# Kernel tuning notes

Hardware: AMD Instinct MI355X
Metric: run time of the kernel (lower is better)

## Reference

```python
import jax, jax.numpy as jnp
import numpy as np
import math

B, T, D, H = 2, 2048, 768, 12
ND = D // H  # head dim = 64


def precompute_freqs_cis(dim, end, theta=10000.0):
    freqs = 1.0 / (theta ** (jnp.arange(0, dim, 2, dtype=jnp.float32) / dim))  # [dim/2]
    t = jnp.arange(end, dtype=jnp.float32)
    freqs = jnp.outer(t, freqs)  # [end, dim/2]
    return jnp.cos(freqs), jnp.sin(freqs)


def apply_rotary_emb(q, k, cos, sin):
    # q, k: [b, t, h, nd]; cos/sin: [t, nd/2]
    def rot(x):
        xr, xi = x[..., 0::2], x[..., 1::2]  # even/odd interleaved split
        c = cos[None, :, None, :]
        s = sin[None, :, None, :]
        out_r = xr * c - xi * s
        out_i = xr * s + xi * c
        return jnp.stack([out_r, out_i], axis=-1).reshape(x.shape)
    return rot(q), rot(k)


def setup_inputs() -> dict:
    key = jax.random.key(0)
    ks = jax.random.split(key, 12)
    sc = 0.02
    q = jax.random.normal(ks[0], (B, T, D), dtype=jnp.float32)
    k = jax.random.normal(ks[1], (B, T, D), dtype=jnp.float32)
    v = jax.random.normal(ks[2], (B, T, D), dtype=jnp.float32)
    mask = jnp.tril(jnp.ones((T, T), dtype=jnp.int32))[None, None]  # causal [1,1,T,T]
    # weights stored as [d_in, d_out] (pre-transposed vs torch Linear)
    wq = jax.random.normal(ks[3], (D, D), dtype=jnp.float32) * sc
    bq = jax.random.normal(ks[4], (D,), dtype=jnp.float32) * sc
    wk = jax.random.normal(ks[5], (D, D), dtype=jnp.float32) * sc
    bk = jax.random.normal(ks[6], (D,), dtype=jnp.float32) * sc
    wv = jax.random.normal(ks[7], (D, D), dtype=jnp.float32) * sc
    bv = jax.random.normal(ks[8], (D,), dtype=jnp.float32) * sc
    wo = jax.random.normal(ks[9], (D, D), dtype=jnp.float32) * sc
    cos, sin = precompute_freqs_cis(ND, T)
    return {"q": q, "k": k, "v": v, "mask": mask, "wq": wq, "bq": bq,
            "wk": wk, "bk": bk, "wv": wv, "bv": bv, "wo": wo,
            "freqs_cos": cos, "freqs_sin": sin}


def reference(q, k, v, mask, wq, bq, wk, bk, wv, bv, wo, freqs_cos, freqs_sin):
    b, t, d = q.shape
    qh = (q @ wq + bq).reshape(b, t, H, ND)
    kh = (k @ wk + bk).reshape(b, t, H, ND)
    vh = (v @ wv + bv).reshape(b, t, H, ND).transpose(0, 2, 1, 3)  # [b,h,t,nd]
    qh, kh = apply_rotary_emb(qh, kh, freqs_cos[:t], freqs_sin[:t])
    qh = qh.transpose(0, 2, 1, 3)  # [b,h,t,nd]
    kh = kh.transpose(0, 2, 1, 3)
    attn = jnp.einsum('bhqd,bhkd->bhqk', qh, kh) / math.sqrt(ND)
    attn = jnp.where(mask == 0, jnp.float32(-jnp.inf), attn)
    probs = jax.nn.softmax(attn, axis=-1)
    out = jnp.einsum('bhqk,bhkd->bhqd', probs, vh)
    out = out.transpose(0, 2, 1, 3).reshape(b, t, d)
    return out @ wo
```

## Files before the change

### kernel.cpp

```cpp
#include <hip/hip_runtime.h>
#include <hip/hip_bf16.h>
#include <math.h>

#define BB 2
#define TT 2048
#define DD 768
#define HH 12
#define ND 64
#define MM (BB*TT)

typedef __attribute__((ext_vector_type(8))) short bf16x8;
typedef __attribute__((ext_vector_type(4))) float f32x4;
typedef __attribute__((ext_vector_type(16))) float f32x16;

__device__ __forceinline__ float bf2f(ushort u) {
    union { unsigned int i; float f; } v; v.i = ((unsigned int)u) << 16; return v.f;
}
__device__ __forceinline__ ushort f2bf(float f) {
    union { float f; unsigned int i; } v; v.f = f;
    unsigned int r = v.i + 0x7FFF + ((v.i >> 16) & 1);
    return (ushort)(r >> 16);
}

__device__ __forceinline__ void cp16(void* lds, const void* g) {
    __builtin_amdgcn_global_load_lds(
        (const __attribute__((address_space(1))) void*)g,
        (__attribute__((address_space(3))) void*)lds, 16, 0, 0);
}

__device__ __forceinline__ float fexp2(float x) {
    float r; asm("v_exp_f32 %0, %1" : "=v"(r) : "v"(x)); return r;
}
__device__ __forceinline__ unsigned int pk_bf16(float a, float b) {
    unsigned int r; asm("v_cvt_pk_bf16_f32 %0, %1, %2" : "=v"(r) : "v"(a), "v"(b)); return r;
}

__device__ __forceinline__ void plswap(unsigned int& a, unsigned int& b) {
#if __has_builtin(__builtin_amdgcn_permlane32_swap)
    auto r = __builtin_amdgcn_permlane32_swap(a, b, false, false);
    a = r[0]; b = r[1];
#else
    unsigned int sa = __shfl_xor((int)a, 32), sb = __shfl_xor((int)b, 32);
    bool hi = (threadIdx.x & 63) >= 32;
    unsigned int na = hi ? sb : a, nb = hi ? b : sa;
    a = na; b = nb;
#endif
}
__device__ __forceinline__ float partner32(float x, int hi) {
#if __has_builtin(__builtin_amdgcn_permlane32_swap)
    unsigned int u = __float_as_uint(x);
    auto r = __builtin_amdgcn_permlane32_swap(u, u, false, false);
    return __uint_as_float(hi ? r[0] : r[1]);
#else
    return __shfl_xor(x, 32);
#endif
}

#define QSCALE 0.18033688011112043f

__global__ void conv_x3(const float* __restrict__ x0, const float* __restrict__ x1,
                        const float* __restrict__ x2,
                        ushort* __restrict__ o0, ushort* __restrict__ o1,
                        ushort* __restrict__ o2)
{
    const float* x = blockIdx.z == 0 ? x0 : (blockIdx.z == 1 ? x1 : x2);
    ushort* o = blockIdx.z == 0 ? o0 : (blockIdx.z == 1 ? o1 : o2);
    int i = (blockIdx.x * 256 + threadIdx.x) * 4;
    if (i >= MM * DD) return;
    float4 v = *(const float4*)&x[i];
    ushort4 r;
    r.x = f2bf(v.x); r.y = f2bf(v.y); r.z = f2bf(v.z); r.w = f2bf(v.w);
    *(ushort4*)&o[i] = r;
}

__global__ __launch_bounds__(256) void conv_wT(const float* __restrict__ w0, const float* __restrict__ w1,
                        const float* __restrict__ w2, const float* __restrict__ w3,
                        ushort* __restrict__ o0, ushort* __restrict__ o1,
                        ushort* __restrict__ o2, ushort* __restrict__ o3)
{
    __shared__ ushort tile[64][72];
    const float* w = blockIdx.z == 0 ? w0 : blockIdx.z == 1 ? w1 : blockIdx.z == 2 ? w2 : w3;
    ushort* o = blockIdx.z == 0 ? o0 : blockIdx.z == 1 ? o1 : blockIdx.z == 2 ? o2 : o3;
    const int k0 = blockIdx.y * 64, n0 = blockIdx.x * 64;
    #pragma unroll
    for (int it = 0; it < 4; ++it) {
        int e = (threadIdx.x + it * 256) * 4;
        int r = e >> 6, c = e & 63;
        float4 v = *(const float4*)&w[(size_t)(k0 + r) * DD + n0 + c];
        tile[c + 0][r] = f2bf(v.x);
        tile[c + 1][r] = f2bf(v.y);
        tile[c + 2][r] = f2bf(v.z);
        tile[c + 3][r] = f2bf(v.w);
    }
    __syncthreads();
    #pragma unroll
    for (int it = 0; it < 4; ++it) {
        int e = (threadIdx.x + it * 256) * 4;
        int nr = e >> 6, kc = e & 63;
        ushort4 r4;
        r4.x = tile[nr][kc + 0];
        r4.y = tile[nr][kc + 1];
        r4.z = tile[nr][kc + 2];
        r4.w = tile[nr][kc + 3];
        *(ushort4*)&o[(size_t)(n0 + nr) * DD + k0 + kc] = r4;
    }
}

struct GArgs { const ushort* x; const ushort* wt; const float* bias; void* out;
               const float* cT; const float* sT; int rope; };

template<int MODE, int TM, int TN>
__global__ __launch_bounds__(256) void gemm_bf16(GArgs a0, GArgs a1, GArgs a2,
                                                 int nx, int ny)
{
    constexpr int WM = TM / 2, WN = TN / 2;
    constexpr int MF = WM / 16, NF = WN / 16;
    constexpr int BUFB = (TM + TN) * 64;
    constexpr int NPASS = BUFB / 4096;
    constexpr int NK = DD / 32;
    __shared__ __align__(16) ushort S[3][BUFB / 2];
    const int tid = threadIdx.x;
    const int w = tid >> 6, l = tid & 63;
    const int wr = w >> 1, wc = w & 1;

    const int G = gridDim.x, per = G >> 3;
    const int p = blockIdx.x;
    const int task = (p & 7) * per + (p >> 3);
    const int bx = task % nx;
    const int by = (task / nx) % ny;
    const int bz = task / (nx * ny);
    GArgs ga = (bz == 0) ? a0 : (bz == 1 ? a1 : a2);
    const int n0 = bx * TN, m0 = by * TM;

    f32x4 acc[MF][NF] = {};

    auto stage = [&](int buf, int k0) {
        #pragma unroll
        for (int it = 0; it < NPASS; ++it) {
            const int ob = it * 4096 + w * 1024;
            const int o = ob + l * 16;
            if (ob < TM * 64) {
                const int row = o >> 6, kb = o & 63;
                cp16((char*)&S[buf][0] + ob,
                     (const char*)ga.x + (size_t)(m0 + row) * (DD * 2) + k0 * 2 + kb);
            } else {
                const int o2 = o - TM * 64;
                const int row = o2 >> 6, kb = o2 & 63;
                cp16((char*)&S[buf][0] + ob,
                     (const char*)ga.wt + (size_t)(n0 + row) * (DD * 2) + k0 * 2 + kb);
            }
        }
    };

    stage(0, 0);
    stage(1, 32);
    if constexpr (NPASS == 2) asm volatile("s_waitcnt vmcnt(2)" ::: "memory");
    else                      asm volatile("s_waitcnt vmcnt(3)" ::: "memory");
    __builtin_amdgcn_s_barrier();

    for (int t = 0; t < NK; ++t) {
        const bool more = (t + 2 < NK);
        if (more) stage((t + 2) % 3, (t + 2) * 32);

        const char* ab = (const char*)&S[t % 3][0];
        bf16x8 af[MF], bfr[NF];
        #pragma unroll
        for (int i = 0; i < MF; ++i)
            af[i] = *(const bf16x8*)(ab + (WM * wr + 16 * i + (l & 15)) * 64 + (l >> 4) * 16);
        #pragma unroll
        for (int j = 0; j < NF; ++j)
            bfr[j] = *(const bf16x8*)(ab + TM * 64 + (WN * wc + 16 * j + (l & 15)) * 64 + (l >> 4) * 16);
        __builtin_amdgcn_s_setprio(1);
        #pragma unroll
        for (int i = 0; i < MF; ++i)
            #pragma unroll
            for (int j = 0; j < NF; ++j)
                acc[i][j] = __builtin_amdgcn_mfma_f32_16x16x32_bf16(af[i], bfr[j], acc[i][j], 0, 0, 0);
        __builtin_amdgcn_s_setprio(0);

        if (more) {
            if constexpr (NPASS == 2) asm volatile("s_waitcnt vmcnt(2)" ::: "memory");
            else                      asm volatile("s_waitcnt vmcnt(3)" ::: "memory");
        } else {
            asm volatile("s_waitcnt vmcnt(0)" ::: "memory");
        }
        __builtin_amdgcn_s_barrier();
    }
    asm volatile("s_waitcnt vmcnt(0)" ::: "memory");

    #pragma unroll
    for (int i = 0; i < MF; ++i) {
        #pragma unroll
        for (int j = 0; j < NF; ++j) {
            #pragma unroll
            for (int r = 0; r < 4; ++r) {
                const int m = m0 + WM * wr + 16 * i + (l >> 4) * 4 + r;
                const int n = n0 + WN * wc + 16 * j + (l & 15);
                float v = acc[i][j][r];
                if (MODE == 0) {
                    v += ga.bias[n];
                    const int tt = m & 2047;
                    if (ga.rope) {
                        const int d = n & 63;
                        const float c = ga.cT[tt * 32 + (d >> 1)];
                        const float s = ga.sT[tt * 32 + (d >> 1)];
                        const float pv = __shfl_xor(v, 1);
                        v = (n & 1) ? (pv * s + v * c) : (v * c - pv * s);
                        if (ga.rope == 2) v *= QSCALE;
                    }
                    const int b = m >> 11;
                    const int h = n >> 6, d = n & 63;
                    ((ushort*)ga.out)[((size_t)(b * HH + h) * TT + tt) * ND + d] = f2bf(v);
                } else {
                    ((float*)ga.out)[(size_t)m * DD + n] = v;
                }
            }
        }
    }
}

__global__ __launch_bounds__(256) void transpose_v(const ushort* __restrict__ Vh,
                                                   ushort* __restrict__ VhT)
{
    __shared__ ushort tile[64][72];
    const int t0 = blockIdx.x * 64, bh = blockIdx.y;
    const ushort* src = Vh + ((size_t)bh * TT + t0) * ND;
    #pragma unroll
    for (int it = 0; it < 4; ++it) {
        int e = (threadIdx.x + it * 256) * 4;
        int r = e >> 6, c = e & 63;
        ushort4 v = *(const ushort4*)&src[r * ND + c];
        tile[r][c + 0] = v.x; tile[r][c + 1] = v.y;
        tile[r][c + 2] = v.z; tile[r][c + 3] = v.w;
    }
    __syncthreads();
    #pragma unroll
    for (int it = 0; it < 4; ++it) {
        int e = (threadIdx.x + it * 256) * 4;
        int d = e >> 6, tc = e & 63;
        ushort4 r4;
        r4.x = tile[tc + 0][d]; r4.y = tile[tc + 1][d];
        r4.z = tile[tc + 2][d]; r4.w = tile[tc + 3][d];
        *(ushort4*)&VhT[((size_t)bh * ND + d) * TT + t0 + tc] = r4;
    }
}

#define NQB (TT/128)
#define NBH (BB*HH)
#define NTASK (NQB*NBH)
#define NCU 256

__global__ __launch_bounds__(512) void attn_mfma4(const ushort* __restrict__ Qh,
                                                  const ushort* __restrict__ Kh,
                                                  const ushort* __restrict__ VhT,
                                                  ushort* __restrict__ Op)
{
    __shared__ __align__(16) ushort Ks[2][2][4096];
    __shared__ __align__(16) ushort Vs[2][2][4096];
    const int tid = threadIdx.x;
    const int w = tid >> 6, l = tid & 63;
    const int lq = l & 31, hi = l >> 5;
    const int qs = w & 3;
    const int kvh = w >> 2;

    const int n = blockIdx.x;
    const int r_ = (n < NCU) ? n : (NTASK - 1 + NCU - n);
    const int qblk = (NQB - 1) - r_ / NBH;
    const int bh = r_ % NBH;

    const int q0 = qblk * 128;
    const int q0w = q0 + qs * 32;
    const int qg = q0w + lq;
    const int ntH = qblk + 1;
    const int kvbase = kvh * ntH * 64;

    const ushort* Qg = Qh + ((size_t)bh * TT + q0w) * ND;
    const ushort* Kg = Kh + (size_t)bh * TT * ND;
    const ushort* Vg = VhT + (size_t)bh * ND * TT;

    bf16x8 qf[4];
    #pragma unroll
    for (int ks = 0; ks < 4; ++ks)
        qf[ks] = *(const bf16x8*)((const char*)Qg + lq * 128 + ks * 32 + hi * 16);

    auto stageKV = [&](int buf, int kv0) {
        #pragma unroll
        for (int it = 0; it < 2; ++it) {
            int o = it * 4096 + qs * 1024 + l * 16;
            int row = o >> 7, inner = o & 127;
            int swz = inner ^ ((row & 7) << 4);
            cp16((char*)&Ks[kvh][buf][0] + it * 4096 + qs * 1024,
                 (const char*)Kg + (size_t)(kv0 + row) * 128 + swz);
            cp16((char*)&Vs[kvh][buf][0] + it * 4096 + qs * 1024,
                 (const char*)Vg + (size_t)row * (TT * 2) + kv0 * 2 + swz);
        }
    };

    float m = -1e30f, lsum = 0.f;
    f32x16 o0 = {}, o1 = {};

    stageKV(0, kvbase);
    __syncthreads();
    for (int t = 0; t < ntH; ++t) {
        const int cur = t & 1;
        if (t + 1 < ntH) stageKV(cur ^ 1, kvbase + (t + 1) * 64);
        const char* kb = (const char*)&Ks[kvh][cur][0];
        const char* vb = (const char*)&Vs[kvh][cur][0];
        const int kvt = kvbase + t * 64;

        if (kvt <= q0w + 31) {
            const bool have1 = (kvt + 32 <= q0w + 31);

            f32x16 st0 = {}, st1 = {};
            __builtin_amdgcn_s_setprio(1);
            #pragma unroll
            for (int ks = 0; ks < 4; ++ks) {
                bf16x8 kf = *(const bf16x8*)(kb + lq * 128 +
                                             ((ks * 32 + hi * 16) ^ ((lq & 7) << 4)));
                st0 = __builtin_amdgcn_mfma_f32_32x32x16_bf16(kf, qf[ks], st0, 0, 0, 0);
            }
            if (have1) {
                #pragma unroll
                for (int ks = 0; ks < 4; ++ks) {
                    bf16x8 kf = *(const bf16x8*)(kb + (32 + lq) * 128 +
                                                 ((ks * 32 + hi * 16) ^ ((lq & 7) << 4)));
                    st1 = __builtin_amdgcn_mfma_f32_32x32x16_bf16(kf, qf[ks], st1, 0, 0, 0);
                }
            }
            __builtin_amdgcn_s_setprio(0);

            float tm = -1e30f;
            if (kvt + 31 > q0w) {
                #pragma unroll
                for (int r = 0; r < 16; ++r) {
                    const int kvg = kvt + (r & 3) + 8 * (r >> 2) + 4 * hi;
                    float x = (kvg <= qg) ? st0[r] : -1e30f;
                    st0[r] = x;
                    tm = fmaxf(tm, x);
                }
            } else {
                #pragma unroll
                for (int r = 0; r < 16; ++r) tm = fmaxf(tm, st0[r]);
            }
            if (have1) {
                if (kvt + 63 > q0w) {
                    #pragma unroll
                    for (int r = 0; r < 16; ++r) {
                        const int kvg = kvt + 32 + (r & 3) + 8 * (r >> 2) + 4 * hi;
                        float x = (kvg <= qg) ? st1[r] : -1e30f;
                        st1[r] = x;
                        tm = fmaxf(tm, x);
                    }
                } else {
                    #pragma unroll
                    for (int r = 0; r < 16; ++r) tm = fmaxf(tm, st1[r]);
                }
            }
            tm = fmaxf(tm, partner32(tm, hi));

            const bool defer = __all(tm <= m + 11.5f);
            float alpha = 1.f;
            if (!defer) {
                const float nm = fmaxf(m, tm);
                alpha = fexp2(m - nm);
                m = nm;
            }

            float ps[16];
            unsigned int pkA[8], pkB[8];
            #pragma unroll
            for (int i = 0; i < 8; ++i) {
                const float p0 = fexp2(st0[2 * i + 0] - m);
                const float p1 = fexp2(st0[2 * i + 1] - m);
                pkA[i] = pk_bf16(p0, p1);
                ps[i] = p0 + p1;
            }
            if (have1) {
                #pragma unroll
                for (int i = 0; i < 8; ++i) {
                    const float p0 = fexp2(st1[2 * i + 0] - m);
                    const float p1 = fexp2(st1[2 * i + 1] - m);
                    pkB[i] = pk_bf16(p0, p1);
                    ps[8 + i] = p0 + p1;
                }
            } else {
                #pragma unroll
                for (int i = 0; i < 8; ++i) { pkB[i] = 0; ps[8 + i] = 0.f; }
            }
            const float t0s = (ps[0] + ps[1]) + (ps[2] + ps[3]);
            const float t1s = (ps[4] + ps[5]) + (ps[6] + ps[7]);
            const float t2s = (ps[8] + ps[9]) + (ps[10] + ps[11]);
            const float t3s = (ps[12] + ps[13]) + (ps[14] + ps[15]);
            float rs = (t0s + t1s) + (t2s + t3s);
            rs += partner32(rs, hi);
            lsum = lsum * alpha + rs;

            plswap(pkA[0], pkA[2]); plswap(pkA[1], pkA[3]);
            plswap(pkA[4], pkA[6]); plswap(pkA[5], pkA[7]);
            if (have1) {
                plswap(pkB[0], pkB[2]); plswap(pkB[1], pkB[3]);
                plswap(pkB[4], pkB[6]); plswap(pkB[5], pkB[7]);
            }
            union { unsigned int u[4]; bf16x8 v; } pa0, pa1, pa2, pa3;
            pa0.u[0] = pkA[0]; pa0.u[1] = pkA[1]; pa0.u[2] = pkA[2]; pa0.u[3] = pkA[3];
            pa1.u[0] = pkA[4]; pa1.u[1] = pkA[5]; pa1.u[2] = pkA[6]; pa1.u[3] = pkA[7];
            pa2.u[0] = pkB[0]; pa2.u[1] = pkB[1]; pa2.u[2] = pkB[2]; pa2.u[3] = pkB[3];
            pa3.u[0] = pkB[4]; pa3.u[1] = pkB[5]; pa3.u[2] = pkB[6]; pa3.u[3] = pkB[7];

            if (!defer) {
                #pragma unroll
                for (int r = 0; r < 16; ++r) { o0[r] *= alpha; o1[r] *= alpha; }
            }

            __builtin_amdgcn_s_setprio(1);
            #pragma unroll
            for (int sl = 0; sl < 2; ++sl) {
                const bf16x8 pf = sl == 0 ? pa0.v : pa1.v;
                const int cb = sl * 32 + hi * 16;
                bf16x8 va = *(const bf16x8*)(vb + lq * 128 + (cb ^ ((lq & 7) << 4)));
                bf16x8 vc = *(const bf16x8*)(vb + (lq + 32) * 128 + (cb ^ ((lq & 7) << 4)));
                o0 = __builtin_amdgcn_mfma_f32_32x32x16_bf16(va, pf, o0, 0, 0, 0);
                o1 = __builtin_amdgcn_mfma_f32_32x32x16_bf16(vc, pf, o1, 0, 0, 0);
            }
            if (have1) {
                #pragma unroll
                for (int sl = 0; sl < 2; ++sl) {
                    const bf16x8 pf = sl == 0 ? pa2.v : pa3.v;
                    const int cb = 64 + sl * 32 + hi * 16;
                    bf16x8 va = *(const bf16x8*)(vb + lq * 128 + (cb ^ ((lq & 7) << 4)));
                    bf16x8 vc = *(const bf16x8*)(vb + (lq + 32) * 128 + (cb ^ ((lq & 7) << 4)));
                    o0 = __builtin_amdgcn_mfma_f32_32x32x16_bf16(va, pf, o0, 0, 0, 0);
                    o1 = __builtin_amdgcn_mfma_f32_32x32x16_bf16(vc, pf, o1, 0, 0, 0);
                }
            }
            __builtin_amdgcn_s_setprio(0);
        }
        __syncthreads();
    }

    float* xO  = (float*)&Ks[0][0][0];
    float* xML = (float*)&Vs[0][0][0];
    if (kvh == 1) {
        float* dst = xO + qs * 2048;
        #pragma unroll
        for (int r = 0; r < 16; ++r) {
            dst[r * 64 + l] = o0[r];
            dst[(r + 16) * 64 + l] = o1[r];
        }
        if (hi == 0) { xML[qs * 64 + lq] = m; xML[qs * 64 + 32 + lq] = lsum; }
    }
    __syncthreads();
    if (kvh == 0) {
        const float* src = xO + qs * 2048;
        const float m1 = xML[qs * 64 + lq];
        const float l1 = xML[qs * 64 + 32 + lq];
        const float ms = fmaxf(m, m1);
        const float a0 = fexp2(m - ms), a1 = fexp2(m1 - ms);
        const float inv = 1.0f / (lsum * a0 + l1 * a1);
        const int b = bh / HH, h = bh % HH;
        ushort* dst = Op + ((size_t)(b * TT + qg)) * DD + h * ND;
        #pragma unroll
        for (int g = 0; g < 4; ++g) {
            ushort4 w0, w1;
            w0.x = f2bf((o0[4 * g + 0] * a0 + src[(4 * g + 0) * 64 + l] * a1) * inv);
            w0.y = f2bf((o0[4 * g + 1] * a0 + src[(4 * g + 1) * 64 + l] * a1) * inv);
            w0.z = f2bf((o0[4 * g + 2] * a0 + src[(4 * g + 2) * 64 + l] * a1) * inv);
            w0.w = f2bf((o0[4 * g + 3] * a0 + src[(4 * g + 3) * 64 + l] * a1) * inv);
            *(ushort4*)&dst[8 * g + 4 * hi] = w0;
            w1.x = f2bf((o1[4 * g + 0] * a0 + src[(16 + 4 * g + 0) * 64 + l] * a1) * inv);
            w1.y = f2bf((o1[4 * g + 1] * a0 + src[(16 + 4 * g + 1) * 64 + l] * a1) * inv);
            w1.z = f2bf((o1[4 * g + 2] * a0 + src[(16 + 4 * g + 2) * 64 + l] * a1) * inv);
            w1.w = f2bf((o1[4 * g + 3] * a0 + src[(16 + 4 * g + 3) * 64 + l] * a1) * inv);
            *(ushort4*)&dst[32 + 8 * g + 4 * hi] = w1;
        }
    }
}

extern "C" void kernel_launch(void* const* d_in, const int* in_sizes, int n_in,
                              void* d_out, int out_size, void* d_ws, size_t ws_size,
                              hipStream_t stream)
{
    const float* q  = (const float*)d_in[0];
    const float* k  = (const float*)d_in[1];
    const float* v  = (const float*)d_in[2];
    const float* wq = (const float*)d_in[4];
    const float* bq = (const float*)d_in[5];
    const float* wk = (const float*)d_in[6];
    const float* bk = (const float*)d_in[7];
    const float* wv = (const float*)d_in[8];
    const float* bv = (const float*)d_in[9];
    const float* wo = (const float*)d_in[10];
    const float* fc = (const float*)d_in[11];
    const float* fs = (const float*)d_in[12];
    float* out = (float*)d_out;

    ushort* qB  = (ushort*)d_ws;
    ushort* kB  = qB  + (size_t)MM * DD;
    ushort* vB  = kB  + (size_t)MM * DD;
    ushort* wqT = vB  + (size_t)MM * DD;
    ushort* wkT = wqT + (size_t)DD * DD;
    ushort* wvT = wkT + (size_t)DD * DD;
    ushort* woT = wvT + (size_t)DD * DD;
    ushort* Qh  = woT + (size_t)DD * DD;
    ushort* Kh  = Qh  + (size_t)MM * DD;
    ushort* Vh  = Kh  + (size_t)MM * DD;
    ushort* VhT = kB;
    ushort* Op  = qB;

    conv_x3<<<dim3(MM * DD / 4 / 256, 1, 3), 256, 0, stream>>>(q, k, v, qB, kB, vB);
    conv_wT<<<dim3(DD / 64, DD / 64, 4), 256, 0, stream>>>(wq, wk, wv, wo, wqT, wkT, wvT, woT);

    GArgs aq{qB, wqT, bq, (void*)Qh, fc, fs, 2};
    GArgs ak{kB, wkT, bk, (void*)Kh, fc, fs, 1};
    GArgs av{vB, wvT, bv, (void*)Vh, nullptr, nullptr, 0};
    gemm_bf16<0, 128, 64><<<dim3(1152), 256, 0, stream>>>(aq, ak, av, DD / 64, MM / 128);

    transpose_v<<<dim3(TT / 64, BB * HH), 256, 0, stream>>>(Vh, VhT);

    attn_mfma4<<<dim3(NTASK), 512, 0, stream>>>(Qh, Kh, VhT, Op);

    GArgs ao{Op, woT, nullptr, (void*)out, nullptr, nullptr, 0};
    gemm_bf16<1, 64, 64><<<dim3(768), 256, 0, stream>>>(ao, ao, ao, DD / 64, MM / 64);
}
```

Measured before the change: 109.8 us.

## Use k-chunk-major LDS layout and double buffering in projection GEMM

Reorganizes the LDS tile layout so each 16-byte k-chunk of all rows is stored contiguously (chunk-major), which should avoid bank conflicts on the bf16x8 fragment reads. At the same time it drops the triple-buffered, vmcnt-controlled pipeline for a double buffer synchronized with __syncthreads. The reduced prefetch depth and full barrier (which waits for all outstanding loads) may expose more global-load latency, but the smaller LDS footprint may improve occupancy.

```diff
diff --git a/kernel.cpp b/kernel.cpp
--- a/kernel.cpp
+++ b/kernel.cpp
@@ -115,10 +115,11 @@
 {
     constexpr int WM = TM / 2, WN = TN / 2;
     constexpr int MF = WM / 16, NF = WN / 16;
+    constexpr int ABYTES = TM * 64;
     constexpr int BUFB = (TM + TN) * 64;
     constexpr int NPASS = BUFB / 4096;
     constexpr int NK = DD / 32;
-    __shared__ __align__(16) ushort S[3][BUFB / 2];
+    __shared__ __align__(16) ushort S[2][BUFB / 2];
     const int tid = threadIdx.x;
     const int w = tid >> 6, l = tid & 63;
     const int wr = w >> 1, wc = w & 1;
@@ -138,38 +139,35 @@
         #pragma unroll
         for (int it = 0; it < NPASS; ++it) {
             const int ob = it * 4096 + w * 1024;
-            const int o = ob + l * 16;
-            if (ob < TM * 64) {
-                const int row = o >> 6, kb = o & 63;
+            if (ob < ABYTES) {
+                const int q = ob / (TM * 16);
+                const int rb = (ob % (TM * 16)) >> 4;
                 cp16((char*)&S[buf][0] + ob,
-                     (const char*)ga.x + (size_t)(m0 + row) * (DD * 2) + k0 * 2 + kb);
+                     (const char*)ga.x + (size_t)(m0 + rb + l) * (DD * 2) + k0 * 2 + q * 16);
             } else {
-                const int o2 = o - TM * 64;
-                const int row = o2 >> 6, kb = o2 & 63;
+                const int ob2 = ob - ABYTES;
+                const int q = ob2 / (TN * 16);
+                const int rb = (ob2 % (TN * 16)) >> 4;
                 cp16((char*)&S[buf][0] + ob,
-                     (const char*)ga.wt + (size_t)(n0 + row) * (DD * 2) + k0 * 2 + kb);
+                     (const char*)ga.wt + (size_t)(n0 + rb + l) * (DD * 2) + k0 * 2 + q * 16);
             }
         }
     };
 
     stage(0, 0);
-    stage(1, 32);
-    if constexpr (NPASS == 2) asm volatile("s_waitcnt vmcnt(2)" ::: "memory");
-    else                      asm volatile("s_waitcnt vmcnt(3)" ::: "memory");
-    __builtin_amdgcn_s_barrier();
-
+    __syncthreads();
     for (int t = 0; t < NK; ++t) {
-        const bool more = (t + 2 < NK);
-        if (more) stage((t + 2) % 3, (t + 2) * 32);
-
-        const char* ab = (const char*)&S[t % 3][0];
+        const int cur = t & 1;
+        if (t + 1 < NK) stage(cur ^ 1, (t + 1) * 32);
+        const char* ab = (const char*)&S[cur][0];
         bf16x8 af[MF], bfr[NF];
+        const int lq = l >> 4, lr = l & 15;
         #pragma unroll
         for (int i = 0; i < MF; ++i)
-            af[i] = *(const bf16x8*)(ab + (WM * wr + 16 * i + (l & 15)) * 64 + (l >> 4) * 16);
+            af[i] = *(const bf16x8*)(ab + lq * (TM * 16) + (WM * wr + 16 * i + lr) * 16);
         #pragma unroll
         for (int j = 0; j < NF; ++j)
-            bfr[j] = *(const bf16x8*)(ab + TM * 64 + (WN * wc + 16 * j + (l & 15)) * 64 + (l >> 4) * 16);
+            bfr[j] = *(const bf16x8*)(ab + ABYTES + lq * (TN * 16) + (WN * wc + 16 * j + lr) * 16);
         __builtin_amdgcn_s_setprio(1);
         #pragma unroll
         for (int i = 0; i < MF; ++i)
@@ -177,16 +175,8 @@
             for (int j = 0; j < NF; ++j)
                 acc[i][j] = __builtin_amdgcn_mfma_f32_16x16x32_bf16(af[i], bfr[j], acc[i][j], 0, 0, 0);
         __builtin_amdgcn_s_setprio(0);
-
-        if (more) {
-            if constexpr (NPASS == 2) asm volatile("s_waitcnt vmcnt(2)" ::: "memory");
-            else                      asm volatile("s_waitcnt vmcnt(3)" ::: "memory");
-        } else {
-            asm volatile("s_waitcnt vmcnt(0)" ::: "memory");
-        }
-        __builtin_amdgcn_s_barrier();
-    }
-    asm volatile("s_waitcnt vmcnt(0)" ::: "memory");
+        __syncthreads();
+    }
 
     #pragma unroll
     for (int i = 0; i < MF; ++i) {
```

Result: slower. 135.3 us (+23.2%).
